# Kernel tuning notes

Hardware: AMD Instinct MI355X
Metric: run time of the kernel (lower is better)

## Reference

```python
import jax, jax.numpy as jnp
import numpy as np

N = 100_000   # nodes
E = 200_000   # directed edges
G = 2_500     # graphs in batch
F_NODE = 16
F_EDGE = 8
H1 = 32
H2 = 16


def setup_inputs() -> dict:
    key = jax.random.key(0)
    ks = jax.random.split(key, 24)
    p = lambda k, shape: 0.1 * jax.random.normal(k, shape, dtype=jnp.float32)
    inp = {
        "x": jax.random.normal(ks[0], (N, F_NODE), dtype=jnp.float32),
        "edge_attr": jax.random.normal(ks[1], (E, F_EDGE), dtype=jnp.float32),
        # edge-MLP for conv1: F_EDGE -> 16 -> F_NODE*H1
        "w_e1a": p(ks[2], (F_EDGE, 16)), "b_e1a": p(ks[3], (16,)),
        "w_e1b": p(ks[4], (16, F_NODE * H1)), "b_e1b": p(ks[5], (F_NODE * H1,)),
        "w_root1": p(ks[6], (F_NODE, H1)), "b_root1": p(ks[7], (H1,)),
        # edge-MLP for conv2: F_EDGE -> 16 -> H1*H2
        "w_e2a": p(ks[8], (F_EDGE, 16)), "b_e2a": p(ks[9], (16,)),
        "w_e2b": p(ks[10], (16, H1 * H2)), "b_e2b": p(ks[11], (H1 * H2,)),
        "w_root2": p(ks[12], (H1, H2)), "b_root2": p(ks[13], (H2,)),
        # attention-pool gate nn: F_NODE -> F_NODE -> 1
        "w_g1": p(ks[14], (F_NODE, F_NODE)), "b_g1": p(ks[15], (F_NODE,)),
        "w_g2": p(ks[16], (F_NODE, 1)), "b_g2": p(ks[17], (1,)),
        # head: (H2 + F_NODE) -> 8 -> 1
        "w_l1": p(ks[18], (H2 + F_NODE, 8)), "b_l1": p(ks[19], (8,)),
        "w_l2": p(ks[20], (8, 1)), "b_l2": p(ks[21], (1,)),
        "edge_index": jax.random.randint(ks[22], (2, E), 0, N),
        "batch": jnp.sort(jax.random.randint(ks[23], (N,), 0, G)),
    }
    return inp


def _nnconv(x, src, tgt, edge_attr, wa, ba, wb, bb, wr, br, in_c, out_c, n):
    # PyG NNConv: x_i' = x_i @ W_root + b + sum_{j->i} x_j @ Theta(e_ji)
    h = jax.nn.relu(edge_attr @ wa + ba)              # [E, 16]
    theta = (h @ wb + bb).reshape(-1, in_c, out_c)    # [E, in, out]
    msg = jnp.einsum('ei,eio->eo', x[src], theta)     # [E, out]
    agg = jax.ops.segment_sum(msg, tgt, num_segments=n)
    return x @ wr + br + agg


def reference(x, edge_attr, w_e1a, b_e1a, w_e1b, b_e1b, w_root1, b_root1,
              w_e2a, b_e2a, w_e2b, b_e2b, w_root2, b_root2,
              w_g1, b_g1, w_g2, b_g2, w_l1, b_l1, w_l2, b_l2,
              edge_index, batch):
    src, tgt = edge_index[0], edge_index[1]
    n = x.shape[0]

    # GlobalAttention pooling on raw node features (per-graph segment softmax)
    gate = jax.nn.relu(x @ w_g1 + b_g1) @ w_g2 + b_g2          # [N, 1]
    m = jax.ops.segment_max(gate, batch, num_segments=G)       # [G, 1]
    a = jnp.exp(gate - m[batch])
    s = jax.ops.segment_sum(a, batch, num_segments=G)
    x_att = jax.ops.segment_sum((a / s[batch]) * x, batch, num_segments=G)  # [G, F_NODE]

    # Two NNConv layers with ReLU
    h = jax.nn.relu(_nnconv(x, src, tgt, edge_attr, w_e1a, b_e1a, w_e1b, b_e1b,
                            w_root1, b_root1, F_NODE, H1, n))
    h = jax.nn.relu(_nnconv(h, src, tgt, edge_attr, w_e2a, b_e2a, w_e2b, b_e2b,
                            w_root2, b_root2, H1, H2, n))

    # global_mean_pool
    cnt = jax.ops.segment_sum(jnp.ones((n, 1), h.dtype), batch, num_segments=G)
    mean = jax.ops.segment_sum(h, batch, num_segments=G) / jnp.maximum(cnt, 1.0)

    z = jnp.concatenate([mean, x_att], axis=1)  # [G, H2 + F_NODE]
    # eval mode: dropout p=0.5 is identity; two linear layers, no activation between
    z = z @ w_l1 + b_l1
    z = z @ w_l2 + b_l2
    return z
```

## Files before the change

### kernel.cpp

```cpp
#include <hip/hip_runtime.h>
#include <hip/hip_bf16.h>

#define NN 100000
#define NE 200000
#define NG 2500
#define FN 16
#define FE 8
#define H1C 32
#define H2C 16
#define KH 16

typedef __attribute__((ext_vector_type(8))) short short8;
typedef __attribute__((ext_vector_type(4))) float f32x4;
typedef _Float16 __attribute__((ext_vector_type(2))) half2v;
typedef _Float16 __attribute__((ext_vector_type(8))) half8v;
typedef __fp16 __attribute__((ext_vector_type(2))) pkf16x2;

__device__ __forceinline__ float bf2f(unsigned int u){
  union { unsigned int i; float f; } v; v.i = (u & 0xffffu) << 16; return v.f;
}
__device__ __forceinline__ unsigned int pkh(float a, float b){
  union { pkf16x2 h; unsigned int u; } v; v.h = __builtin_amdgcn_cvt_pkrtz(a, b); return v.u;
}
__device__ __forceinline__ float h2lo(unsigned int u){
  union { unsigned short s; _Float16 h; } v; v.s = (unsigned short)u; return (float)v.h;
}
__device__ __forceinline__ float h2hi(unsigned int u){
  union { unsigned short s; _Float16 h; } v; v.s = (unsigned short)(u >> 16); return (float)v.h;
}
__device__ __forceinline__ float rdf(const void* p, long i, bool isbf){
  return isbf ? bf2f(((const unsigned short*)p)[i]) : ((const float*)p)[i];
}
__device__ __forceinline__ void atomic_pk_f16(unsigned short* addr, unsigned int pk){
  asm volatile("global_atomic_pk_add_f16 %0, %1, off" :: "v"(addr), "v"(pk) : "memory");
}
__device__ __forceinline__ bool detect_isbf(const void* __restrict__ x){
  const unsigned short* u = (const unsigned short*)x;
  int lane = threadIdx.x & 63;
  float f = bf2f(u[2*lane]);
  float a = fabsf(f);
  bool sane = (f == 0.0f) || (a > 1e-4f && a < 1e4f);
  unsigned long long b = __ballot(sane);
  return __popcll(b) >= 32;
}

#define NW 20
struct WArgs { const void* p[NW]; };
enum {
  OW_E1A=0,     OB_E1A=128,   OW_E1B=144,   OB_E1B=8336,  OW_R1=8848,  OB_R1=9360,
  OW_E2A=9392,  OB_E2A=9520,  OW_E2B=9536,  OB_E2B=17728, OW_R2=18240, OB_R2=18752,
  OW_G1=18768,  OB_G1=19024,  OW_G2=19040,  OB_G2=19056,
  OW_L1=19057,  OB_L1=19313,  OW_L2=19321,  OB_L2=19329
};

#define MB_A 76
#define MB_B (MB_A + 19)
#define MB_C (MB_B + 18)
#define MB_D (MB_C + 391)
#define MB_E (MB_D + 782)
__global__ void __launch_bounds__(256) mega1_kernel(
    const void* __restrict__ xin, const void* __restrict__ efin, WArgs w,
    const int* __restrict__ batch,
    float* __restrict__ wts, unsigned int* __restrict__ wpack1, unsigned int* __restrict__ wpack2,
    float* __restrict__ gate, float* __restrict__ xf,
    unsigned int* __restrict__ hpk1, unsigned int* __restrict__ hpk2,
    int* __restrict__ gstart)
{
  int b = blockIdx.x, tid = threadIdx.x;
  if(b < MB_A){
    bool isbf = detect_isbf(xin);
    int i = b*256 + tid;
    if(i >= 19330) return;
    const int sz[NW] = {128,16,8192,512,512,32, 128,16,8192,512,512,16, 256,16,16,1, 256,8,8,1};
    int seg = 0; long base = 0;
    while(i - base >= sz[seg]){ base += sz[seg]; seg++; }
    wts[i] = rdf(w.p[seg], i - base, isbf);
    return;
  }
  if(b < MB_B){
    bool isbf = detect_isbf(xin);
    int j = (b - MB_A)*256 + tid;
    if(j >= 4736) return;
    int n = j / 148; int k = (j % 148) * 2;
    float v0 = 0.f, v1 = 0.f;
    if(k < 256)        v0 = rdf(w.p[2], (long)k*32 + n, isbf);
    else if(k < 272)   v0 = rdf(w.p[3], (long)(k-256)*32 + n, isbf);
    if(k+1 < 256)      v1 = rdf(w.p[2], (long)(k+1)*32 + n, isbf);
    else if(k+1 < 272) v1 = rdf(w.p[3], (long)(k+1-256)*32 + n, isbf);
    wpack1[j] = pkh(v0, v1);
    return;
  }
  if(b < MB_C){
    bool isbf = detect_isbf(xin);
    int j = (b - MB_B)*256 + tid;
    if(j >= 4416) return;
    int n = j / 276; int k = (j % 276) * 2;
    float v0 = 0.f, v1 = 0.f;
    if(k < 512)        v0 = rdf(w.p[8], (long)k*16 + n, isbf);
    else if(k < 544)   v0 = rdf(w.p[9], (long)(k-512)*16 + n, isbf);
    if(k+1 < 512)      v1 = rdf(w.p[8], (long)(k+1)*16 + n, isbf);
    else if(k+1 < 544) v1 = rdf(w.p[9], (long)(k+1-512)*16 + n, isbf);
    wpack2[j] = pkh(v0, v1);
    return;
  }
  if(b < MB_D){
    __shared__ float s_w1[FN*FN], s_b1[FN], s_w2[FN], s_b2v[1];
    bool isbf = detect_isbf(xin);
    if(tid < FN*FN) s_w1[tid] = rdf(w.p[12], tid, isbf);
    if(tid < FN){ s_b1[tid] = rdf(w.p[13], tid, isbf); s_w2[tid] = rdf(w.p[14], tid, isbf); }
    if(tid == 0) s_b2v[0] = rdf(w.p[15], 0, isbf);
    __syncthreads();
    int n = (b - MB_C)*256 + tid;
    if(n >= NN) return;
    {
      int b1 = batch[n];
      int b0 = (n == 0) ? -1 : batch[n-1];
      for(int g2 = b0 + 1; g2 <= b1; g2++) gstart[g2] = n;
      if(n == NN-1) for(int g2 = b1 + 1; g2 <= NG; g2++) gstart[g2] = NN;
    }
    float xv[FN];
    if(isbf){
      uint4 u0 = ((const uint4*)xin)[2*n], u1 = ((const uint4*)xin)[2*n+1];
      xv[0]=bf2f(u0.x); xv[1]=bf2f(u0.x>>16); xv[2]=bf2f(u0.y); xv[3]=bf2f(u0.y>>16);
      xv[4]=bf2f(u0.z); xv[5]=bf2f(u0.z>>16); xv[6]=bf2f(u0.w); xv[7]=bf2f(u0.w>>16);
      xv[8]=bf2f(u1.x); xv[9]=bf2f(u1.x>>16); xv[10]=bf2f(u1.y); xv[11]=bf2f(u1.y>>16);
      xv[12]=bf2f(u1.z); xv[13]=bf2f(u1.z>>16); xv[14]=bf2f(u1.w); xv[15]=bf2f(u1.w>>16);
    } else {
      #pragma unroll
      for(int q = 0; q < 4; q++){
        float4 v = ((const float4*)xin)[4*n + q];
        xv[q*4+0]=v.x; xv[q*4+1]=v.y; xv[q*4+2]=v.z; xv[q*4+3]=v.w;
      }
    }
    float4* xo = (float4*)(xf + (size_t)n*FN);
    #pragma unroll
    for(int q = 0; q < 4; q++) xo[q] = make_float4(xv[q*4+0], xv[q*4+1], xv[q*4+2], xv[q*4+3]);
    float g = s_b2v[0];
    #pragma unroll
    for(int j = 0; j < FN; j++){
      float hj = s_b1[j];
      #pragma unroll
      for(int i = 0; i < FN; i++) hj += xv[i] * s_w1[i*FN + j];
      hj = hj > 0.f ? hj : 0.f;
      g += hj * s_w2[j];
    }
    gate[n] = g;
    return;
  }
  {
    __shared__ float s_w1[FE*KH], s_b1[KH], s_w2[FE*KH], s_b2[KH];
    bool isbf = detect_isbf(xin);
    if(tid < FE*KH){ s_w1[tid] = rdf(w.p[0], tid, isbf); s_w2[tid] = rdf(w.p[6], tid, isbf); }
    if(tid < KH){ s_b1[tid] = rdf(w.p[1], tid, isbf); s_b2[tid] = rdf(w.p[7], tid, isbf); }
    __syncthreads();
    int e = (b - MB_D)*256 + tid;
    if(e >= NE) return;
    float ev[FE];
    if(isbf){
      uint4 u = ((const uint4*)efin)[e];
      ev[0]=bf2f(u.x); ev[1]=bf2f(u.x>>16); ev[2]=bf2f(u.y); ev[3]=bf2f(u.y>>16);
      ev[4]=bf2f(u.z); ev[5]=bf2f(u.z>>16); ev[6]=bf2f(u.w); ev[7]=bf2f(u.w>>16);
    } else {
      float4 a = ((const float4*)efin)[2*e], bb = ((const float4*)efin)[2*e+1];
      ev[0]=a.x; ev[1]=a.y; ev[2]=a.z; ev[3]=a.w; ev[4]=bb.x; ev[5]=bb.y; ev[6]=bb.z; ev[7]=bb.w;
    }
    unsigned int o[8];
    #pragma unroll
    for(int d = 0; d < 8; d++){
      float h0 = s_b1[2*d], h1 = s_b1[2*d+1];
      #pragma unroll
      for(int k = 0; k < FE; k++){
        h0 += ev[k] * s_w1[k*KH + 2*d];
        h1 += ev[k] * s_w1[k*KH + 2*d+1];
      }
      h0 = h0 > 0.f ? h0 : 0.f; h1 = h1 > 0.f ? h1 : 0.f;
      o[d] = pkh(h0, h1);
    }
    uint4* p1 = (uint4*)(hpk1 + (size_t)e*8);
    p1[0] = make_uint4(o[0],o[1],o[2],o[3]); p1[1] = make_uint4(o[4],o[5],o[6],o[7]);
    #pragma unroll
    for(int d = 0; d < 8; d++){
      float h0 = s_b2[2*d], h1 = s_b2[2*d+1];
      #pragma unroll
      for(int k = 0; k < FE; k++){
        h0 += ev[k] * s_w2[k*KH + 2*d];
        h1 += ev[k] * s_w2[k*KH + 2*d+1];
      }
      h0 = h0 > 0.f ? h0 : 0.f; h1 = h1 > 0.f ? h1 : 0.f;
      o[d] = pkh(h0, h1);
    }
    uint4* p2 = (uint4*)(hpk2 + (size_t)e*8);
    p2[0] = make_uint4(o[0],o[1],o[2],o[3]); p2[1] = make_uint4(o[4],o[5],o[6],o[7]);
  }
}

template<int IN, int OUT, bool AH>
__global__ void __launch_bounds__(256) conv_atomic_kernel(
    const void* __restrict__ nodef, const unsigned int* __restrict__ hpk,
    const int* __restrict__ ei, const unsigned short* __restrict__ wpack,
    unsigned short* __restrict__ agg)
{
  constexpr int KMF  = ((KH*IN + IN + 31)/32)*32;
  constexpr int KP   = KMF + 8;
  constexpr int NT   = OUT/16;
  constexpr int KS   = KMF/32;
  int tid = threadIdx.x;
  int lane = tid & 63, m = lane & 15, quad = lane >> 4;
  int wid = tid >> 6;
  int ebase = blockIdx.x*64 + wid*16;
  int em = ebase + m;
  int sn = ei[em];
  int q1 = quad >> 1;
  int xoff = (IN == 16) ? ((quad & 1)*8) : (quad*8);
  union { half8v v; half2v h[4]; unsigned int w[4]; } X;
  if(AH){
    uint4 u = *(const uint4*)((const unsigned short*)nodef + (size_t)sn*IN + xoff);
    X.w[0]=u.x; X.w[1]=u.y; X.w[2]=u.z; X.w[3]=u.w;
  } else {
    const float4* xp = (const float4*)((const float*)nodef + (size_t)sn*IN + xoff);
    float4 v0 = xp[0], v1 = xp[1];
    X.w[0] = pkh(v0.x, v0.y);
    X.w[1] = pkh(v0.z, v0.w);
    X.w[2] = pkh(v1.x, v1.y);
    X.w[3] = pkh(v1.z, v1.w);
  }
  unsigned int hu[8];
  {
    const uint4* hp = (const uint4*)(hpk + (size_t)em*8);
    uint4 u0 = hp[0], u1 = hp[1];
    hu[0]=u0.x; hu[1]=u0.y; hu[2]=u0.z; hu[3]=u0.w;
    hu[4]=u1.x; hu[5]=u1.y; hu[6]=u1.z; hu[7]=u1.w;
  }
  int4 tg = *(const int4*)(ei + NE + ebase + quad*4);

  f32x4 acc[NT];
  #pragma unroll
  for(int nt = 0; nt < NT; nt++) acc[nt] = (f32x4){0.f,0.f,0.f,0.f};

  const half8v hz = {};
  #pragma unroll
  for(int ks = 0; ks < KS; ks++){
    union { half8v v; half2v h[4]; } A;
    if(ks < KS-1){
      unsigned short hs = (unsigned short)((IN == 16) ? (hu[ks] >> (16*q1))
                                                      : (hu[ks >> 1] >> (16*(ks & 1))));
      union { unsigned short s; _Float16 h; } hc; hc.s = hs;
      half2v hv2 = { hc.h, hc.h };
      #pragma unroll
      for(int k = 0; k < 4; k++) A.h[k] = hv2 * X.h[k];
    } else {
      if(IN == 16) A.v = (quad < 2) ? X.v : hz;
      else         A.v = X.v;
    }
    #pragma unroll
    for(int nt = 0; nt < NT; nt++){
      half8v b = *(const half8v*)(wpack + (size_t)(nt*16 + m)*KP + ks*32 + quad*8);
      acc[nt] = __builtin_amdgcn_mfma_f32_16x16x32_f16(A.v, b, acc[nt], 0, 0, 0);
    }
  }
  int tr[4] = {tg.x, tg.y, tg.z, tg.w};
  int mlo = m & ~1;
  bool evn = (m & 1) == 0;
  #pragma unroll
  for(int r = 0; r < 4; r++){
    #pragma unroll
    for(int nt = 0; nt < NT; nt++){
      float v = acc[nt][r];
      float vn = __shfl_xor(v, 1);
      if(evn ? (r < 2) : (r >= 2)){
        unsigned int pk = evn ? pkh(v, vn) : pkh(vn, v);
        atomic_pk_f16(agg + (size_t)tr[r]*OUT + nt*16 + mlo, pk);
      }
    }
  }
}

__global__ void __launch_bounds__(256) node1_kernel(
    const float* __restrict__ xf, const unsigned short* __restrict__ agg1,
    const float* __restrict__ wr, const float* __restrict__ br,
    unsigned short* __restrict__ h1b)
{
  __shared__ float s_w[FN*H1C], s_b[H1C];
  for(int i = threadIdx.x; i < FN*H1C; i += 256) s_w[i] = wr[i];
  if(threadIdx.x < H1C) s_b[threadIdx.x] = br[threadIdx.x];
  __syncthreads();
  int g = blockIdx.x*256 + threadIdx.x;
  int n = g >> 3, q = g & 7;
  if(n >= NN) return;
  uint2 au = *(const uint2*)(agg1 + (size_t)n*H1C + q*4);
  float a0 = s_b[q*4+0] + h2lo(au.x), a1 = s_b[q*4+1] + h2hi(au.x);
  float a2 = s_b[q*4+2] + h2lo(au.y), a3 = s_b[q*4+3] + h2hi(au.y);
  const float* xr = xf + (size_t)n*FN;
  #pragma unroll
  for(int i = 0; i < FN; i++){
    float xi = xr[i];
    a0 += xi*s_w[i*H1C + q*4+0]; a1 += xi*s_w[i*H1C + q*4+1];
    a2 += xi*s_w[i*H1C + q*4+2]; a3 += xi*s_w[i*H1C + q*4+3];
  }
  a0 = a0>0.f?a0:0.f; a1 = a1>0.f?a1:0.f; a2 = a2>0.f?a2:0.f; a3 = a3>0.f?a3:0.f;
  uint2 hb; hb.x = pkh(a0, a1); hb.y = pkh(a2, a3);
  *(uint2*)(h1b + (size_t)n*H1C + q*4) = hb;
}

__global__ void __launch_bounds__(256) node2_kernel(
    const unsigned short* __restrict__ h1b, const unsigned short* __restrict__ agg2,
    const float* __restrict__ wr, const float* __restrict__ br, float* __restrict__ h2)
{
  __shared__ float s_w[H1C*H2C], s_b[H2C];
  for(int i = threadIdx.x; i < H1C*H2C; i += 256) s_w[i] = wr[i];
  if(threadIdx.x < H2C) s_b[threadIdx.x] = br[threadIdx.x];
  __syncthreads();
  int g = blockIdx.x*256 + threadIdx.x;
  int n = g >> 2, q = g & 3;
  if(n >= NN) return;
  uint2 au = *(const uint2*)(agg2 + (size_t)n*H2C + q*4);
  float a0 = s_b[q*4+0] + h2lo(au.x), a1 = s_b[q*4+1] + h2hi(au.x);
  float a2 = s_b[q*4+2] + h2lo(au.y), a3 = s_b[q*4+3] + h2hi(au.y);
  const unsigned int* hb = (const unsigned int*)(h1b + (size_t)n*H1C);
  #pragma unroll
  for(int i2 = 0; i2 < H1C/2; i2++){
    unsigned int u = hb[i2];
    float x0 = h2lo(u), x1 = h2hi(u);
    int i = 2*i2;
    a0 += x0*s_w[i*H2C + q*4+0] + x1*s_w[(i+1)*H2C + q*4+0];
    a1 += x0*s_w[i*H2C + q*4+1] + x1*s_w[(i+1)*H2C + q*4+1];
    a2 += x0*s_w[i*H2C + q*4+2] + x1*s_w[(i+1)*H2C + q*4+2];
    a3 += x0*s_w[i*H2C + q*4+3] + x1*s_w[(i+1)*H2C + q*4+3];
  }
  float4 r; r.x = a0>0.f?a0:0.f; r.y = a1>0.f?a1:0.f; r.z = a2>0.f?a2:0.f; r.w = a3>0.f?a3:0.f;
  *(float4*)(h2 + (size_t)n*H2C + q*4) = r;
}

__global__ void head_kernel(const float* __restrict__ gate, const float* __restrict__ xf,
    const float* __restrict__ h2, const int* __restrict__ gstart, const void* __restrict__ xin,
    const float* __restrict__ wl1, const float* __restrict__ bl1,
    const float* __restrict__ wl2, const float* __restrict__ bl2,
    void* __restrict__ out)
{
  __shared__ float sz[H2C + FN];
  int g = blockIdx.x;
  int lane = threadIdx.x;
  bool isbf = detect_isbf(xin);
  int start = gstart[g];
  int end   = gstart[g + 1];
  float m = -1e30f;
  for(int n = start + lane; n < end; n += 64) m = fmaxf(m, gate[n]);
  #pragma unroll
  for(int o = 32; o >= 1; o >>= 1) m = fmaxf(m, __shfl_xor(m, o));
  float s = 0.f;
  float acc[FN];
  #pragma unroll
  for(int f = 0; f < FN; f++) acc[f] = 0.f;
  for(int n = start + lane; n < end; n += 64){
    float a = __expf(gate[n] - m);
    s += a;
    const float4* xp = (const float4*)(xf + (size_t)n * FN);
    #pragma unroll
    for(int q = 0; q < 4; q++){
      float4 v = xp[q];
      acc[q*4+0] += a*v.x; acc[q*4+1] += a*v.y; acc[q*4+2] += a*v.z; acc[q*4+3] += a*v.w;
    }
  }
  #pragma unroll
  for(int o = 32; o >= 1; o >>= 1){
    s += __shfl_xor(s, o);
    #pragma unroll
    for(int f = 0; f < FN; f++) acc[f] += __shfl_xor(acc[f], o);
  }
  if(lane < FN) sz[H2C + lane] = (end > start && s > 0.f) ? acc[lane] / s : 0.f;
  #pragma unroll
  for(int f = 0; f < H2C; f++) acc[f] = 0.f;
  for(int n = start + lane; n < end; n += 64){
    const float4* hp = (const float4*)(h2 + (size_t)n*H2C);
    #pragma unroll
    for(int q = 0; q < 4; q++){
      float4 v = hp[q];
      acc[q*4+0] += v.x; acc[q*4+1] += v.y; acc[q*4+2] += v.z; acc[q*4+3] += v.w;
    }
  }
  #pragma unroll
  for(int o = 32; o >= 1; o >>= 1){
    #pragma unroll
    for(int f = 0; f < H2C; f++) acc[f] += __shfl_xor(acc[f], o);
  }
  float inv = 1.f / fmaxf((float)(end - start), 1.f);
  if(lane < H2C) sz[lane] = acc[lane] * inv;
  __syncthreads();
  if(lane == 0){
    float t1[8];
    #pragma unroll
    for(int j = 0; j < 8; j++){
      float t = bl1[j];
      #pragma unroll
      for(int c = 0; c < H2C + FN; c++) t += sz[c] * wl1[c*8 + j];
      t1[j] = t;
    }
    float o = bl2[0];
    #pragma unroll
    for(int j = 0; j < 8; j++) o += t1[j] * wl2[j];
    if(isbf) ((__hip_bfloat16*)out)[g] = __float2bfloat16(o);
    else     ((float*)out)[g] = o;
  }
}

extern "C" void kernel_launch(void* const* d_in, const int* in_sizes, int n_in,
                              void* d_out, int out_size, void* d_ws, size_t ws_size,
                              hipStream_t stream)
{
  const int* ei    = (const int*)d_in[22];
  const int* batch = (const int*)d_in[23];

  float* ws = (float*)d_ws;
  float* xf     = ws;
  float* gate   = xf + 1600000;
  float* wts    = gate + 100000;
  int*   gstart = (int*)(wts + 19360);
  unsigned int* wpack1 = (unsigned int*)(gstart + 2504);
  unsigned int* wpack2 = wpack1 + 4736;
  unsigned int* hpk1   = wpack2 + 4416;
  unsigned int* hpk2   = hpk1 + 1600000;
  unsigned short* h1b  = (unsigned short*)(hpk2 + 1600000);
  float* h2     = (float*)(h1b + 3200000);
  unsigned short* agg1 = (unsigned short*)(h2 + 1600000);
  unsigned short* agg2 = agg1 + 3200000;

  WArgs wa;
  for(int i = 0; i < NW; i++) wa.p[i] = d_in[2 + i];

  hipMemsetAsync(agg1, 0, (size_t)(3200000 + 1600000)*sizeof(unsigned short), stream);
  mega1_kernel<<<MB_E, 256, 0, stream>>>(d_in[0], d_in[1], wa, batch,
      wts, wpack1, wpack2, gate, xf, hpk1, hpk2, gstart);

  conv_atomic_kernel<FN, H1C, false><<<NE/64, 256, 0, stream>>>(
      xf, hpk1, ei, (const unsigned short*)wpack1, agg1);
  node1_kernel<<<(NN*8 + 255)/256, 256, 0, stream>>>(xf, agg1, wts+OW_R1, wts+OB_R1, h1b);

  conv_atomic_kernel<H1C, H2C, true><<<NE/64, 256, 0, stream>>>(
      h1b, hpk2, ei, (const unsigned short*)wpack2, agg2);
  node2_kernel<<<(NN*4 + 255)/256, 256, 0, stream>>>(h1b, agg2, wts+OW_R2, wts+OB_R2, h2);

  head_kernel<<<NG, 64, 0, stream>>>(gate, xf, h2, gstart, d_in[0],
      wts+OW_L1, wts+OB_L1, wts+OW_L2, wts+OB_L2, d_out);
}
```

Baseline: 189.6 us.

## Fuse edge-MLP first layer into conv kernels instead of precomputing hidden buffers

Removes the edge-MLP hidden-layer stage from the first mega kernel and recomputes each edge's relu(edge_attr @ W_a + b_a) inside each conv kernel from shared-memory weights. This drops writing and rereading two E×16 fp16 intermediate buffers and shrinks the prologue kernel. In exchange each conv kernel rereads edge_attr and does extra per-lane FMAs, and the weight permutation for the IN=16 case must match the lane's k-slice.

```diff
diff --git a/kernel.cpp b/kernel.cpp
--- a/kernel.cpp
+++ b/kernel.cpp
@@ -57,13 +57,11 @@
 #define MB_B (MB_A + 19)
 #define MB_C (MB_B + 18)
 #define MB_D (MB_C + 391)
-#define MB_E (MB_D + 782)
 __global__ void __launch_bounds__(256) mega1_kernel(
-    const void* __restrict__ xin, const void* __restrict__ efin, WArgs w,
+    const void* __restrict__ xin, WArgs w,
     const int* __restrict__ batch,
     float* __restrict__ wts, unsigned int* __restrict__ wpack1, unsigned int* __restrict__ wpack2,
     float* __restrict__ gate, float* __restrict__ xf,
-    unsigned int* __restrict__ hpk1, unsigned int* __restrict__ hpk2,
     int* __restrict__ gstart)
 {
   int b = blockIdx.x, tid = threadIdx.x;
@@ -103,7 +101,7 @@
     wpack2[j] = pkh(v0, v1);
     return;
   }
-  if(b < MB_D){
+  {
     __shared__ float s_w1[FN*FN], s_b1[FN], s_w2[FN], s_b2v[1];
     bool isbf = detect_isbf(xin);
     if(tid < FN*FN) s_w1[tid] = rdf(w.p[12], tid, isbf);
@@ -145,58 +143,13 @@
       g += hj * s_w2[j];
     }
     gate[n] = g;
-    return;
-  }
-  {
-    __shared__ float s_w1[FE*KH], s_b1[KH], s_w2[FE*KH], s_b2[KH];
-    bool isbf = detect_isbf(xin);
-    if(tid < FE*KH){ s_w1[tid] = rdf(w.p[0], tid, isbf); s_w2[tid] = rdf(w.p[6], tid, isbf); }
-    if(tid < KH){ s_b1[tid] = rdf(w.p[1], tid, isbf); s_b2[tid] = rdf(w.p[7], tid, isbf); }
-    __syncthreads();
-    int e = (b - MB_D)*256 + tid;
-    if(e >= NE) return;
-    float ev[FE];
-    if(isbf){
-      uint4 u = ((const uint4*)efin)[e];
-      ev[0]=bf2f(u.x); ev[1]=bf2f(u.x>>16); ev[2]=bf2f(u.y); ev[3]=bf2f(u.y>>16);
-      ev[4]=bf2f(u.z); ev[5]=bf2f(u.z>>16); ev[6]=bf2f(u.w); ev[7]=bf2f(u.w>>16);
-    } else {
-      float4 a = ((const float4*)efin)[2*e], bb = ((const float4*)efin)[2*e+1];
-      ev[0]=a.x; ev[1]=a.y; ev[2]=a.z; ev[3]=a.w; ev[4]=bb.x; ev[5]=bb.y; ev[6]=bb.z; ev[7]=bb.w;
-    }
-    unsigned int o[8];
-    #pragma unroll
-    for(int d = 0; d < 8; d++){
-      float h0 = s_b1[2*d], h1 = s_b1[2*d+1];
-      #pragma unroll
-      for(int k = 0; k < FE; k++){
-        h0 += ev[k] * s_w1[k*KH + 2*d];
-        h1 += ev[k] * s_w1[k*KH + 2*d+1];
-      }
-      h0 = h0 > 0.f ? h0 : 0.f; h1 = h1 > 0.f ? h1 : 0.f;
-      o[d] = pkh(h0, h1);
-    }
-    uint4* p1 = (uint4*)(hpk1 + (size_t)e*8);
-    p1[0] = make_uint4(o[0],o[1],o[2],o[3]); p1[1] = make_uint4(o[4],o[5],o[6],o[7]);
-    #pragma unroll
-    for(int d = 0; d < 8; d++){
-      float h0 = s_b2[2*d], h1 = s_b2[2*d+1];
-      #pragma unroll
-      for(int k = 0; k < FE; k++){
-        h0 += ev[k] * s_w2[k*KH + 2*d];
-        h1 += ev[k] * s_w2[k*KH + 2*d+1];
-      }
-      h0 = h0 > 0.f ? h0 : 0.f; h1 = h1 > 0.f ? h1 : 0.f;
-      o[d] = pkh(h0, h1);
-    }
-    uint4* p2 = (uint4*)(hpk2 + (size_t)e*8);
-    p2[0] = make_uint4(o[0],o[1],o[2],o[3]); p2[1] = make_uint4(o[4],o[5],o[6],o[7]);
   }
 }
 
 template<int IN, int OUT, bool AH>
 __global__ void __launch_bounds__(256) conv_atomic_kernel(
-    const void* __restrict__ nodef, const unsigned int* __restrict__ hpk,
+    const void* __restrict__ nodef, const void* __restrict__ efin, const void* __restrict__ xin,
+    const float* __restrict__ wts,
     const int* __restrict__ ei, const unsigned short* __restrict__ wpack,
     unsigned short* __restrict__ agg)
 {
@@ -204,7 +157,22 @@
   constexpr int KP   = KMF + 8;
   constexpr int NT   = OUT/16;
   constexpr int KS   = KMF/32;
+  constexpr int NH   = KS - 1;
+  constexpr int OWA  = (IN == 16) ? OW_E1A : OW_E2A;
+  constexpr int OBA  = (IN == 16) ? OB_E1A : OB_E2A;
+  __shared__ float s_w[FE*KH], s_b[KH];
   int tid = threadIdx.x;
+  if(tid < FE*KH){
+    int k = tid / KH, j = tid % KH;
+    int jj = (IN == 16) ? ((j & 1)*8 + (j >> 1)) : j;
+    s_w[k*KH + jj] = wts[OWA + tid];
+  }
+  if(tid < KH){
+    int jj = (IN == 16) ? ((tid & 1)*8 + (tid >> 1)) : tid;
+    s_b[jj] = wts[OBA + tid];
+  }
+  bool isbf = detect_isbf(xin);
+  __syncthreads();
   int lane = tid & 63, m = lane & 15, quad = lane >> 4;
   int wid = tid >> 6;
   int ebase = blockIdx.x*64 + wid*16;
@@ -224,13 +192,29 @@
     X.w[2] = pkh(v1.x, v1.y);
     X.w[3] = pkh(v1.z, v1.w);
   }
-  unsigned int hu[8];
-  {
-    const uint4* hp = (const uint4*)(hpk + (size_t)em*8);
-    uint4 u0 = hp[0], u1 = hp[1];
-    hu[0]=u0.x; hu[1]=u0.y; hu[2]=u0.z; hu[3]=u0.w;
-    hu[4]=u1.x; hu[5]=u1.y; hu[6]=u1.z; hu[7]=u1.w;
-  }
+  float ev[FE];
+  if(isbf){
+    uint4 u = ((const uint4*)efin)[em];
+    ev[0]=bf2f(u.x); ev[1]=bf2f(u.x>>16); ev[2]=bf2f(u.y); ev[3]=bf2f(u.y>>16);
+    ev[4]=bf2f(u.z); ev[5]=bf2f(u.z>>16); ev[6]=bf2f(u.w); ev[7]=bf2f(u.w>>16);
+  } else {
+    float4 a = ((const float4*)efin)[2*em], bb = ((const float4*)efin)[2*em+1];
+    ev[0]=a.x; ev[1]=a.y; ev[2]=a.z; ev[3]=a.w; ev[4]=bb.x; ev[5]=bb.y; ev[6]=bb.z; ev[7]=bb.w;
+  }
+  int hbase = (IN == 16) ? q1*8 : 0;
+  float hv[NH];
+  #pragma unroll
+  for(int t = 0; t < NH; t++) hv[t] = s_b[hbase + t];
+  #pragma unroll
+  for(int k = 0; k < FE; k++){
+    float evk = ev[k];
+    #pragma unroll
+    for(int t = 0; t < NH; t++) hv[t] += evk * s_w[k*KH + hbase + t];
+  }
+  _Float16 hf[NH];
+  #pragma unroll
+  for(int t = 0; t < NH; t++) hf[t] = (_Float16)(hv[t] > 0.f ? hv[t] : 0.f);
+
   int4 tg = *(const int4*)(ei + NE + ebase + quad*4);
 
   f32x4 acc[NT];
@@ -242,10 +226,7 @@
   for(int ks = 0; ks < KS; ks++){
     union { half8v v; half2v h[4]; } A;
     if(ks < KS-1){
-      unsigned short hs = (unsigned short)((IN == 16) ? (hu[ks] >> (16*q1))
-                                                      : (hu[ks >> 1] >> (16*(ks & 1))));
-      union { unsigned short s; _Float16 h; } hc; hc.s = hs;
-      half2v hv2 = { hc.h, hc.h };
+      half2v hv2 = { hf[ks], hf[ks] };
       #pragma unroll
       for(int k = 0; k < 4; k++) A.h[k] = hv2 * X.h[k];
     } else {
@@ -417,9 +398,7 @@
   int*   gstart = (int*)(wts + 19360);
   unsigned int* wpack1 = (unsigned int*)(gstart + 2504);
   unsigned int* wpack2 = wpack1 + 4736;
-  unsigned int* hpk1   = wpack2 + 4416;
-  unsigned int* hpk2   = hpk1 + 1600000;
-  unsigned short* h1b  = (unsigned short*)(hpk2 + 1600000);
+  unsigned short* h1b  = (unsigned short*)(wpack2 + 4416);
   float* h2     = (float*)(h1b + 3200000);
   unsigned short* agg1 = (unsigned short*)(h2 + 1600000);
   unsigned short* agg2 = agg1 + 3200000;
@@ -428,15 +407,15 @@
   for(int i = 0; i < NW; i++) wa.p[i] = d_in[2 + i];
 
   hipMemsetAsync(agg1, 0, (size_t)(3200000 + 1600000)*sizeof(unsigned short), stream);
-  mega1_kernel<<<MB_E, 256, 0, stream>>>(d_in[0], d_in[1], wa, batch,
-      wts, wpack1, wpack2, gate, xf, hpk1, hpk2, gstart);
+  mega1_kernel<<<MB_D, 256, 0, stream>>>(d_in[0], wa, batch,
+      wts, wpack1, wpack2, gate, xf, gstart);
 
   conv_atomic_kernel<FN, H1C, false><<<NE/64, 256, 0, stream>>>(
-      xf, hpk1, ei, (const unsigned short*)wpack1, agg1);
+      xf, d_in[1], d_in[0], wts, ei, (const unsigned short*)wpack1, agg1);
   node1_kernel<<<(NN*8 + 255)/256, 256, 0, stream>>>(xf, agg1, wts+OW_R1, wts+OB_R1, h1b);
 
   conv_atomic_kernel<H1C, H2C, true><<<NE/64, 256, 0, stream>>>(
-      h1b, hpk2, ei, (const unsigned short*)wpack2, agg2);
+      h1b, d_in[1], d_in[0], wts, ei, (const unsigned short*)wpack2, agg2);
   node2_kernel<<<(NN*4 + 255)/256, 256, 0, stream>>>(h1b, agg2, wts+OW_R2, wts+OB_R2, h2);
 
   head_kernel<<<NG, 64, 0, stream>>>(gate, xf, h2, gstart, d_in[0],
```

Result: slower. 196.3 us (+3.5%).

## Fold accumulator zeroing into prep kernel and attention pooling into conv1

Applied to the files above, without the earlier changes.

Removes the separate memset by adding extra blocks to the first prep kernel that zero the agg1/agg2 accumulators. The per-graph attention-pool softmax reduction moves out of the head kernel into extra blocks of the first conv kernel, where it writes x_att to a new workspace buffer. This cuts one launch and lets the pooling overlap the atomic-heavy conv1 work, leaving the head kernel with only the mean pool. The cost is a heavier prep kernel and a workspace layout shift to make room for x_att.

```diff
diff --git a/kernel.cpp b/kernel.cpp
--- a/kernel.cpp
+++ b/kernel.cpp
@@ -10,7 +10,6 @@
 #define H2C 16
 #define KH 16
 
-typedef __attribute__((ext_vector_type(8))) short short8;
 typedef __attribute__((ext_vector_type(4))) float f32x4;
 typedef _Float16 __attribute__((ext_vector_type(2))) half2v;
 typedef _Float16 __attribute__((ext_vector_type(8))) half8v;
@@ -58,13 +57,14 @@
 #define MB_C (MB_B + 18)
 #define MB_D (MB_C + 391)
 #define MB_E (MB_D + 782)
+#define MB_F (MB_E + 586)
 __global__ void __launch_bounds__(256) mega1_kernel(
     const void* __restrict__ xin, const void* __restrict__ efin, WArgs w,
     const int* __restrict__ batch,
     float* __restrict__ wts, unsigned int* __restrict__ wpack1, unsigned int* __restrict__ wpack2,
     float* __restrict__ gate, float* __restrict__ xf,
     unsigned int* __restrict__ hpk1, unsigned int* __restrict__ hpk2,
-    int* __restrict__ gstart)
+    int* __restrict__ gstart, unsigned short* __restrict__ agg1)
 {
   int b = blockIdx.x, tid = threadIdx.x;
   if(b < MB_A){
@@ -147,7 +147,7 @@
     gate[n] = g;
     return;
   }
-  {
+  if(b < MB_E){
     __shared__ float s_w1[FE*KH], s_b1[KH], s_w2[FE*KH], s_b2[KH];
     bool isbf = detect_isbf(xin);
     if(tid < FE*KH){ s_w1[tid] = rdf(w.p[0], tid, isbf); s_w2[tid] = rdf(w.p[6], tid, isbf); }
@@ -191,15 +191,59 @@
     }
     uint4* p2 = (uint4*)(hpk2 + (size_t)e*8);
     p2[0] = make_uint4(o[0],o[1],o[2],o[3]); p2[1] = make_uint4(o[4],o[5],o[6],o[7]);
-  }
-}
-
-template<int IN, int OUT, bool AH>
+    return;
+  }
+  {
+    int idx = (b - MB_E)*256 + tid;
+    if(idx < 150000){
+      uint4 z = make_uint4(0,0,0,0);
+      uint4* p = (uint4*)((char*)agg1 + (size_t)idx*64);
+      p[0] = z; p[1] = z; p[2] = z; p[3] = z;
+    }
+  }
+}
+
+#define CONV_NB (NE/64)
+#define ATT_NB  (NG/4)
+template<int IN, int OUT, bool AH, bool ATT>
 __global__ void __launch_bounds__(256) conv_atomic_kernel(
     const void* __restrict__ nodef, const unsigned int* __restrict__ hpk,
     const int* __restrict__ ei, const unsigned short* __restrict__ wpack,
-    unsigned short* __restrict__ agg)
-{
+    unsigned short* __restrict__ agg,
+    const float* __restrict__ gate, const float* __restrict__ xf,
+    const int* __restrict__ gstart, float* __restrict__ xatt)
+{
+  if(ATT && blockIdx.x >= CONV_NB){
+    int lane = threadIdx.x & 63, wid = threadIdx.x >> 6;
+    int g = (blockIdx.x - CONV_NB)*4 + wid;
+    int start = gstart[g], end = gstart[g+1];
+    float mx = -1e30f;
+    for(int n = start + lane; n < end; n += 64) mx = fmaxf(mx, gate[n]);
+    #pragma unroll
+    for(int o = 32; o >= 1; o >>= 1) mx = fmaxf(mx, __shfl_xor(mx, o));
+    float s = 0.f;
+    float acc[FN];
+    #pragma unroll
+    for(int f = 0; f < FN; f++) acc[f] = 0.f;
+    for(int n = start + lane; n < end; n += 64){
+      float a = __expf(gate[n] - mx);
+      s += a;
+      const float4* xp = (const float4*)(xf + (size_t)n * FN);
+      #pragma unroll
+      for(int q = 0; q < 4; q++){
+        float4 v = xp[q];
+        acc[q*4+0] += a*v.x; acc[q*4+1] += a*v.y; acc[q*4+2] += a*v.z; acc[q*4+3] += a*v.w;
+      }
+    }
+    #pragma unroll
+    for(int o = 32; o >= 1; o >>= 1){
+      s += __shfl_xor(s, o);
+      #pragma unroll
+      for(int f = 0; f < FN; f++) acc[f] += __shfl_xor(acc[f], o);
+    }
+    if(lane < FN) xatt[(size_t)g*FN + lane] = (end > start && s > 0.f) ? acc[lane] / s : 0.f;
+    return;
+  }
   constexpr int KMF  = ((KH*IN + IN + 31)/32)*32;
   constexpr int KP   = KMF + 8;
   constexpr int NT   = OUT/16;
@@ -331,7 +375,7 @@
   *(float4*)(h2 + (size_t)n*H2C + q*4) = r;
 }
 
-__global__ void head_kernel(const float* __restrict__ gate, const float* __restrict__ xf,
+__global__ void head_kernel(const float* __restrict__ xatt,
     const float* __restrict__ h2, const int* __restrict__ gstart, const void* __restrict__ xin,
     const float* __restrict__ wl1, const float* __restrict__ bl1,
     const float* __restrict__ wl2, const float* __restrict__ bl2,
@@ -343,31 +387,7 @@
   bool isbf = detect_isbf(xin);
   int start = gstart[g];
   int end   = gstart[g + 1];
-  float m = -1e30f;
-  for(int n = start + lane; n < end; n += 64) m = fmaxf(m, gate[n]);
-  #pragma unroll
-  for(int o = 32; o >= 1; o >>= 1) m = fmaxf(m, __shfl_xor(m, o));
-  float s = 0.f;
-  float acc[FN];
-  #pragma unroll
-  for(int f = 0; f < FN; f++) acc[f] = 0.f;
-  for(int n = start + lane; n < end; n += 64){
-    float a = __expf(gate[n] - m);
-    s += a;
-    const float4* xp = (const float4*)(xf + (size_t)n * FN);
-    #pragma unroll
-    for(int q = 0; q < 4; q++){
-      float4 v = xp[q];
-      acc[q*4+0] += a*v.x; acc[q*4+1] += a*v.y; acc[q*4+2] += a*v.z; acc[q*4+3] += a*v.w;
-    }
-  }
-  #pragma unroll
-  for(int o = 32; o >= 1; o >>= 1){
-    s += __shfl_xor(s, o);
-    #pragma unroll
-    for(int f = 0; f < FN; f++) acc[f] += __shfl_xor(acc[f], o);
-  }
-  if(lane < FN) sz[H2C + lane] = (end > start && s > 0.f) ? acc[lane] / s : 0.f;
+  float acc[H2C];
   #pragma unroll
   for(int f = 0; f < H2C; f++) acc[f] = 0.f;
   for(int n = start + lane; n < end; n += 64){
@@ -385,6 +405,7 @@
   }
   float inv = 1.f / fmaxf((float)(end - start), 1.f);
   if(lane < H2C) sz[lane] = acc[lane] * inv;
+  if(lane < FN)  sz[H2C + lane] = xatt[(size_t)g*FN + lane];
   __syncthreads();
   if(lane == 0){
     float t1[8];
@@ -414,7 +435,8 @@
   float* xf     = ws;
   float* gate   = xf + 1600000;
   float* wts    = gate + 100000;
-  int*   gstart = (int*)(wts + 19360);
+  float* xatt   = wts + 19360;
+  int*   gstart = (int*)(xatt + 40000);
   unsigned int* wpack1 = (unsigned int*)(gstart + 2504);
   unsigned int* wpack2 = wpack1 + 4736;
   unsigned int* hpk1   = wpack2 + 4416;
@@ -427,18 +449,17 @@
   WArgs wa;
   for(int i = 0; i < NW; i++) wa.p[i] = d_in[2 + i];
 
-  hipMemsetAsync(agg1, 0, (size_t)(3200000 + 1600000)*sizeof(unsigned short), stream);
-  mega1_kernel<<<MB_E, 256, 0, stream>>>(d_in[0], d_in[1], wa, batch,
-      wts, wpack1, wpack2, gate, xf, hpk1, hpk2, gstart);
-
-  conv_atomic_kernel<FN, H1C, false><<<NE/64, 256, 0, stream>>>(
-      xf, hpk1, ei, (const unsigned short*)wpack1, agg1);
+  mega1_kernel<<<MB_F, 256, 0, stream>>>(d_in[0], d_in[1], wa, batch,
+      wts, wpack1, wpack2, gate, xf, hpk1, hpk2, gstart, agg1);
+
+  conv_atomic_kernel<FN, H1C, false, true><<<CONV_NB + ATT_NB, 256, 0, stream>>>(
+      xf, hpk1, ei, (const unsigned short*)wpack1, agg1, gate, xf, gstart, xatt);
   node1_kernel<<<(NN*8 + 255)/256, 256, 0, stream>>>(xf, agg1, wts+OW_R1, wts+OB_R1, h1b);
 
-  conv_atomic_kernel<H1C, H2C, true><<<NE/64, 256, 0, stream>>>(
-      h1b, hpk2, ei, (const unsigned short*)wpack2, agg2);
+  conv_atomic_kernel<H1C, H2C, true, false><<<CONV_NB, 256, 0, stream>>>(
+      h1b, hpk2, ei, (const unsigned short*)wpack2, agg2, gate, xf, gstart, xatt);
   node2_kernel<<<(NN*4 + 255)/256, 256, 0, stream>>>(h1b, agg2, wts+OW_R2, wts+OB_R2, h2);
 
-  head_kernel<<<NG, 64, 0, stream>>>(gate, xf, h2, gstart, d_in[0],
+  head_kernel<<<NG, 64, 0, stream>>>(xatt, h2, gstart, d_in[0],
       wts+OW_L1, wts+OB_L1, wts+OW_L2, wts+OB_L2, d_out);
 }
```

Result: no change. 186.8 us (-1.5%).
